# Optimization experiments

Measured on AMD Instinct MI355X. Metric: run time of the kernel, lower is better.

## Reference

```python
import jax, jax.numpy as jnp
import numpy as np

B, S, D = 8, 4096, 1024
H, DH = 16, 64
DM = H * DH  # d_model = 1024


def setup_inputs() -> dict:
    key = jax.random.key(0)
    k0, k1, k2, k3 = jax.random.split(key, 4)
    x = jax.random.uniform(k0, (B, S, D), dtype=jnp.float32)
    # nn.Linear weights (stored here pre-transposed as [in, out]).
    Wq = jax.random.normal(k1, (D, DM), dtype=jnp.float32) * 0.02
    Wkv = jax.random.normal(k2, (D, 2 * DM), dtype=jnp.float32) * 0.02
    Wlin = jax.random.normal(k3, (DM, DM), dtype=jnp.float32) * 0.02
    blin = jnp.zeros((DM,), dtype=jnp.float32)
    return {"x": x, "Wq": Wq, "Wkv": Wkv, "Wlin": Wlin, "blin": blin}


def reference(x, Wq, Wkv, Wlin, blin):
    scale = DH ** (-0.5)
    # projections; cond_dim=None => cond = x (self attention), mask=None
    q = (x @ Wq).reshape(B, S, H, DH)          # [B,S,H,DH]
    kv = (x @ Wkv).reshape(B, S, H, 2 * DH)    # [B,S,H,2*DH]
    k, v = kv[..., :DH], kv[..., DH:]
    # dual softmax: q over feature dim (scaled), k over sequence dim
    q = jax.nn.softmax(q, axis=-1) * scale
    k = jax.nn.softmax(k, axis=1)              # seq axis in BSHD layout
    # context = k^T @ v per (batch, head): [B,H,DH,DH]
    context = jnp.einsum('bshd,bshe->bhde', k, v)
    # out = q @ context: [B,S,H,DH]
    out = jnp.einsum('bshd,bhde->bshe', q, context).reshape(B, S, DM)
    return out @ Wlin + blin
```

## Files before the change

kernel.cpp:

```cpp
#include <hip/hip_runtime.h>
#include <hip/hip_bf16.h>
#include <cstdint>

using bf16 = __hip_bfloat16;
typedef __attribute__((ext_vector_type(8))) short bf16x8;
typedef __attribute__((ext_vector_type(4))) float f32x4;

struct alignas(16) B8 { bf16 h[8]; };
struct alignas(8)  B4 { bf16 h[4]; };

__device__ __forceinline__ void gll16(const void* g, void* l) {
  __builtin_amdgcn_global_load_lds((__attribute__((address_space(1))) void*)g,
                                   (__attribute__((address_space(3))) void*)l,
                                   16, 0, 0);
}

__global__ void cast_f32_bf16(const float* __restrict__ in, bf16* __restrict__ out, long long n) {
  long long i = ((long long)blockIdx.x * blockDim.x + threadIdx.x) * 8;
  if (i >= n) return;
  float4 v0 = *(const float4*)(in + i);
  float4 v1 = *(const float4*)(in + i + 4);
  B8 o;
  o.h[0] = __float2bfloat16(v0.x); o.h[1] = __float2bfloat16(v0.y);
  o.h[2] = __float2bfloat16(v0.z); o.h[3] = __float2bfloat16(v0.w);
  o.h[4] = __float2bfloat16(v1.x); o.h[5] = __float2bfloat16(v1.y);
  o.h[6] = __float2bfloat16(v1.z); o.h[7] = __float2bfloat16(v1.w);
  *(B8*)(out + i) = o;
}

__global__ void tcast(const float* __restrict__ W, bf16* __restrict__ WT, int K, int N) {
  __shared__ float tile[32][33];
  int k0 = blockIdx.y * 32, n0 = blockIdx.x * 32;
  int tx = threadIdx.x, ty = threadIdx.y;
  for (int yy = ty; yy < 32; yy += 8)
    tile[yy][tx] = W[(size_t)(k0 + yy) * N + n0 + tx];
  __syncthreads();
  for (int yy = ty; yy < 32; yy += 8)
    WT[(size_t)(n0 + yy) * K + k0 + tx] = __float2bfloat16(tile[tx][yy]);
}

__device__ __forceinline__ void gemm_mainloop_256(
    const bf16* __restrict__ aop0, const bf16* __restrict__ aop1,
    const bf16* __restrict__ bop0, const bf16* __restrict__ bop1,
    bf16* ldsA, bf16* ldsB, int wd0, int wd1,
    int aoff, int boff, f32x4 (&acc)[8][4])
{
#define STAGE_A(slot, ko) do { gll16(aop0 + (ko), ldsA + (slot) * 8192 + wd0); \
                               gll16(aop1 + (ko), ldsA + (slot) * 8192 + wd1); } while (0)
#define STAGE_B(slot, ko) do { gll16(bop0 + (ko), ldsB + (slot) * 8192 + wd0); \
                               gll16(bop1 + (ko), ldsB + (slot) * 8192 + wd1); } while (0)
#define AFRAG(slot, i) (*(const bf16x8*)(ldsA + (slot) * 8192 + aoff + (i) * 512))
#define BFRAG(slot, j) (*(const bf16x8*)(ldsB + (slot) * 8192 + boff + (j) * 512))

  bf16x8 a1[4], a2[4], bb[2][4];

#define SECTION(S, CURB, NXTB, DO_PF, PFS)                                          \
  do {                                                                              \
    asm volatile("s_waitcnt lgkmcnt(0)" ::: "memory");                              \
    __builtin_amdgcn_sched_barrier(0);                                              \
    __builtin_amdgcn_s_setprio(1);                                                  \
    _Pragma("unroll")                                                               \
    for (int i = 0; i < 4; i++) {                                                   \
      _Pragma("unroll")                                                             \
      for (int j = 0; j < 4; j++)                                                   \
        acc[i][j] = __builtin_amdgcn_mfma_f32_16x16x32_bf16(a1[i], bb[CURB][j],     \
                                                            acc[i][j], 0, 0, 0);    \
      a2[i] = AFRAG(S, i + 4);                                                      \
    }                                                                               \
    asm volatile("s_waitcnt lgkmcnt(0)" ::: "memory");                              \
    __builtin_amdgcn_sched_barrier(0);                                              \
    _Pragma("unroll")                                                               \
    for (int i = 0; i < 4; i++) {                                                   \
      _Pragma("unroll")                                                             \
      for (int j = 0; j < 4; j++)                                                   \
        acc[i + 4][j] = __builtin_amdgcn_mfma_f32_16x16x32_bf16(a2[i], bb[CURB][j], \
                                                                acc[i + 4][j], 0, 0, 0); \
      if (DO_PF) { bb[NXTB][i] = BFRAG(PFS, i); a1[i] = AFRAG(PFS, i); }            \
    }                                                                               \
    __builtin_amdgcn_s_setprio(0);                                                  \
  } while (0)

#define BOUNDARY(VMC, DO_STAGE, SLOT, KO)                                           \
  do {                                                                              \
    asm volatile("s_waitcnt vmcnt(" #VMC ")" ::: "memory");                         \
    __builtin_amdgcn_s_barrier();                                                   \
    __builtin_amdgcn_sched_barrier(0);                                              \
    if (DO_STAGE) { STAGE_A(SLOT, KO); STAGE_B(SLOT, KO); }                         \
  } while (0)

  STAGE_A(0, 0);  STAGE_B(0, 0);
  STAGE_A(1, 32); STAGE_B(1, 32);
  STAGE_A(2, 64); STAGE_B(2, 64);
  asm volatile("s_waitcnt vmcnt(8)" ::: "memory");
  __builtin_amdgcn_s_barrier();
  __builtin_amdgcn_sched_barrier(0);
  STAGE_A(3, 96); STAGE_B(3, 96);
  #pragma unroll
  for (int j = 0; j < 4; j++) bb[0][j] = BFRAG(0, j);
  #pragma unroll
  for (int i = 0; i < 4; i++) a1[i] = AFRAG(0, i);

  for (int q = 0; q < 7; ++q) {
    const int ko = q * 128 + 128;
    SECTION(0, 0, 1, true, 1);
    BOUNDARY(4, true, 0, ko);
    SECTION(1, 1, 0, true, 2);
    BOUNDARY(4, true, 1, ko + 32);
    SECTION(2, 0, 1, true, 3);
    BOUNDARY(4, true, 2, ko + 64);
    SECTION(3, 1, 0, true, 0);
    BOUNDARY(4, true, 3, ko + 96);
  }
  SECTION(0, 0, 1, true, 1);
  BOUNDARY(4, false, 0, 0);
  SECTION(1, 1, 0, true, 2);
  BOUNDARY(0, false, 0, 0);
  SECTION(2, 0, 1, true, 3);
  BOUNDARY(0, false, 0, 0);
  SECTION(3, 1, 0, false, 0);

  __syncthreads();
#undef SECTION
#undef BOUNDARY
#undef STAGE_A
#undef STAGE_B
#undef AFRAG
#undef BFRAG
}

constexpr int QKV_NT = 12;

__global__ __launch_bounds__(512, 2)
void gemm_qkv(const bf16* __restrict__ A, const bf16* __restrict__ BT,
              bf16* __restrict__ Yq, float* __restrict__ ctxAcc)
{
  __shared__ __align__(16) union {
    struct { bf16 a[4 * 8192]; bf16 b[4 * 8192]; } g;
    struct { bf16 ekT[2][16384]; bf16 vT[2][16384]; } c;
  } sm;

  const int t = threadIdx.x;
  const int wave = t >> 6, lane = t & 63;
  const int lr = lane & 15, kq = lane >> 4;
  const int wm = wave >> 2, wn = wave & 3;
  const int bid = (int)blockIdx.x;
  const int swz = (bid & 7) * 192 + (bid >> 3);
  const int bm = swz / QKV_NT, bn = swz % QKV_NT;
  const int m0 = bm * 256, n0 = bn * 256;

  const bf16* aop0 = A + (size_t)(m0 + wave * 16 + lr) * 1024 + kq * 8;
  const bf16* aop1 = A + (size_t)(m0 + 128 + wave * 16 + lr) * 1024 + kq * 8;
  const bf16* bop0 = BT + (size_t)(n0 + wave * 16 + lr) * 1024 + kq * 8;
  const bf16* bop1 = BT + (size_t)(n0 + 128 + wave * 16 + lr) * 1024 + kq * 8;
  const int wd0 = wave * 512;
  const int wd1 = 4096 + wave * 512;

  const int aoff = wm * 4096 + lane * 8;
  const int boff = wn * 2048 + lane * 8;

  const f32x4 zero = {0.f, 0.f, 0.f, 0.f};
  f32x4 acc[8][4];
  #pragma unroll
  for (int i = 0; i < 8; i++)
    #pragma unroll
    for (int j = 0; j < 4; j++) acc[i][j] = zero;

  gemm_mainloop_256(aop0, aop1, bop0, bop1, sm.g.a, sm.g.b, wd0, wd1,
                    aoff, boff, acc);

  if (bn < 4) {
    #pragma unroll
    for (int i = 0; i < 8; i++) {
      #pragma unroll
      for (int r = 0; r < 4; r++) {
        float m = fmaxf(fmaxf(acc[i][0][r], acc[i][1][r]),
                        fmaxf(acc[i][2][r], acc[i][3][r]));
        m = fmaxf(m, __shfl_xor(m, 1));
        m = fmaxf(m, __shfl_xor(m, 2));
        m = fmaxf(m, __shfl_xor(m, 4));
        m = fmaxf(m, __shfl_xor(m, 8));
        float ex[4]; float s = 0.f;
        #pragma unroll
        for (int j = 0; j < 4; j++) { ex[j] = __expf(acc[i][j][r] - m); s += ex[j]; }
        s += __shfl_xor(s, 1);
        s += __shfl_xor(s, 2);
        s += __shfl_xor(s, 4);
        s += __shfl_xor(s, 8);
        const float inv = 0.125f / s;
        const int row = m0 + wm * 128 + i * 16 + kq * 4 + r;
        bf16* yrow = Yq + (size_t)row * 1024 + n0 + wn * 64;
        #pragma unroll
        for (int j = 0; j < 4; j++)
          yrow[j * 16 + lr] = __float2bfloat16(ex[j] * inv);
      }
    }
  } else {
    const int bb2 = m0 >> 12;
    const int h0 = (n0 - 1024) >> 7;
    const int hloc = wn >> 1, isV = wn & 1;
    bf16* const dstT = (isV ? sm.c.vT[hloc] : sm.c.ekT[hloc]);

    float zp[4] = {0.f, 0.f, 0.f, 0.f};
    #pragma unroll
    for (int i = 0; i < 8; i++) {
      const int sbase = wm * 128 + i * 16 + kq * 4;
      const int sxo = sbase >> 3;
      const int sby = (sbase & 7) * 2;
      #pragma unroll
      for (int j = 0; j < 4; j++) {
        const int d = j * 16 + lr;
        B4 pk;
        if (!isV) {
          #pragma unroll
          for (int r = 0; r < 4; r++) {
            float e = __expf(acc[i][j][r]);
            zp[j] += e;
            pk.h[r] = __float2bfloat16(e);
          }
        } else {
          #pragma unroll
          for (int r = 0; r < 4; r++) pk.h[r] = __float2bfloat16(acc[i][j][r]);
        }
        *(B4*)((char*)dstT + d * 512 + ((sxo ^ (d & 7)) << 4) + sby) = pk;
      }
    }

    if (!isV) {
      #pragma unroll
      for (int j = 0; j < 4; j++) {
        zp[j] += __shfl_xor(zp[j], 16);
        zp[j] += __shfl_xor(zp[j], 32);
      }
      if (kq == 0) {
        float* zb = ctxAcc + (size_t)(bb2 * 16 + h0 + hloc) * 4160 + 4096;
        #pragma unroll
        for (int j = 0; j < 4; j++) atomicAdd(zb + j * 16 + lr, zp[j]);
      }
    }
    __syncthreads();

    const int hh = wave >> 2, dq = wave & 3;
    const bf16* const ek = sm.c.ekT[hh];
    const bf16* const vv = sm.c.vT[hh];
    f32x4 racc[4] = {zero, zero, zero, zero};
    #pragma unroll
    for (int ks = 0; ks < 8; ks++) {
      const int ch = ks * 4 + kq;
      bf16x8 af = *(const bf16x8*)((const char*)ek + (dq * 16 + lr) * 512 + ((ch ^ (lr & 7)) << 4));
      #pragma unroll
      for (int j = 0; j < 4; j++) {
        bf16x8 bfr = *(const bf16x8*)((const char*)vv + (j * 16 + lr) * 512 + ((ch ^ (lr & 7)) << 4));
        racc[j] = __builtin_amdgcn_mfma_f32_16x16x32_bf16(af, bfr, racc[j], 0, 0, 0);
      }
    }
    float* cb = ctxAcc + (size_t)(bb2 * 16 + h0 + hh) * 4160;
    #pragma unroll
    for (int j = 0; j < 4; j++) {
      #pragma unroll
      for (int r = 0; r < 4; r++)
        atomicAdd(cb + (dq * 16 + kq * 4 + r) * 64 + j * 16 + lr, racc[j][r]);
    }
  }
}

__global__ __launch_bounds__(256) void make_w2t(const float* __restrict__ ctxAcc,
                                                const bf16* __restrict__ WlinT,
                                                bf16* __restrict__ W2T) {
  const int nc = blockIdx.x;
  const int bh = blockIdx.y;
  const int b = bh >> 4, h = bh & 15;
  const int t = threadIdx.x, lane = t & 63, w = t >> 6;
  const float* src = ctxAcc + (size_t)bh * 4160;
  const float invz = 1.0f / src[4096 + lane];
  float creg[64];
  const float* crow = src + lane * 64;
  #pragma unroll
  for (int e4 = 0; e4 < 16; e4++) {
    float4 v = *(const float4*)(crow + e4 * 4);
    creg[e4 * 4 + 0] = v.x * invz; creg[e4 * 4 + 1] = v.y * invz;
    creg[e4 * 4 + 2] = v.z * invz; creg[e4 * 4 + 3] = v.w * invz;
  }
  for (int i = 0; i < 16; i++) {
    const int n = nc * 64 + w * 16 + i;
    const bf16* wrow = WlinT + (size_t)n * 1024 + h * 64;
    float acc = 0.f;
    #pragma unroll
    for (int e8 = 0; e8 < 8; e8++) {
      B8 v = *(const B8*)(wrow + e8 * 8);
      #pragma unroll
      for (int j = 0; j < 8; j++) acc += creg[e8 * 8 + j] * __bfloat162float(v.h[j]);
    }
    W2T[((size_t)b * 1024 + n) * 1024 + h * 64 + lane] = __float2bfloat16(acc);
  }
}

__global__ __launch_bounds__(512, 2)
void gemm_out(const bf16* __restrict__ Aall, const bf16* __restrict__ BTall,
              float* __restrict__ Call, const float* __restrict__ bias)
{
  __shared__ __align__(16) struct { bf16 a[4 * 8192]; bf16 b[4 * 8192]; } sm;
  const int t = threadIdx.x;
  const int wave = t >> 6, lane = t & 63;
  const int lr = lane & 15, kq = lane >> 4;
  const int wm = wave >> 2, wn = wave & 3;
  const int bid = (int)blockIdx.x;
  const int swz = (bid & 7) * 64 + (bid >> 3);
  const int bz = swz >> 6;
  const int r  = swz & 63;
  const int bm = r >> 2, bn = r & 3;
  const int m0 = bm * 256, n0 = bn * 256;
  const bf16* A  = Aall  + (size_t)bz * 4096 * 1024;
  const bf16* BT = BTall + (size_t)bz * 1024 * 1024;
  float* C       = Call  + (size_t)bz * 4096 * 1024;

  const bf16* aop0 = A + (size_t)(m0 + wave * 16 + lr) * 1024 + kq * 8;
  const bf16* aop1 = A + (size_t)(m0 + 128 + wave * 16 + lr) * 1024 + kq * 8;
  const bf16* bop0 = BT + (size_t)(n0 + wave * 16 + lr) * 1024 + kq * 8;
  const bf16* bop1 = BT + (size_t)(n0 + 128 + wave * 16 + lr) * 1024 + kq * 8;
  const int wd0 = wave * 512;
  const int wd1 = 4096 + wave * 512;

  const int aoff = wm * 4096 + lane * 8;
  const int boff = wn * 2048 + lane * 8;

  const f32x4 zero = {0.f, 0.f, 0.f, 0.f};
  f32x4 acc[8][4];
  #pragma unroll
  for (int i = 0; i < 8; i++)
    #pragma unroll
    for (int j = 0; j < 4; j++) acc[i][j] = zero;

  gemm_mainloop_256(aop0, aop1, bop0, bop1, sm.a, sm.b, wd0, wd1,
                    aoff, boff, acc);

  float bv[4];
  #pragma unroll
  for (int j = 0; j < 4; j++) bv[j] = bias[n0 + wn * 64 + j * 16 + lr];
  #pragma unroll
  for (int i = 0; i < 8; i++) {
    const int row0 = m0 + wm * 128 + i * 16 + kq * 4;
    #pragma unroll
    for (int j = 0; j < 4; j++) {
      const int col = n0 + wn * 64 + j * 16 + lr;
      const float bvj = bv[j];
      #pragma unroll
      for (int r2 = 0; r2 < 4; r2++)
        C[(size_t)(row0 + r2) * 1024 + col] = acc[i][j][r2] + bvj;
    }
  }
}

extern "C" void kernel_launch(void* const* d_in, const int* in_sizes, int n_in,
                              void* d_out, int out_size, void* d_ws, size_t ws_size,
                              hipStream_t stream) {
  (void)in_sizes; (void)n_in; (void)out_size; (void)ws_size;
  const float* x    = (const float*)d_in[0];
  const float* Wq   = (const float*)d_in[1];
  const float* Wkv  = (const float*)d_in[2];
  const float* Wlin = (const float*)d_in[3];
  const float* blin = (const float*)d_in[4];
  float* out = (float*)d_out;

  bf16* x_bf  = (bf16*)d_ws;
  bf16* WTc   = x_bf + 33554432;
  bf16* WlinT = WTc + 3145728;
  bf16* Yq    = WlinT + 1048576;
  bf16* W2T   = Yq + 33554432;
  float* ctxAcc = (float*)(W2T + 8388608);

  cast_f32_bf16<<<16384, 256, 0, stream>>>(x, x_bf, 33554432LL);
  tcast<<<dim3(32, 32), dim3(32, 8), 0, stream>>>(Wq, WTc, 1024, 1024);
  tcast<<<dim3(64, 32), dim3(32, 8), 0, stream>>>(Wkv, WTc + 1048576, 1024, 2048);
  tcast<<<dim3(32, 32), dim3(32, 8), 0, stream>>>(Wlin, WlinT, 1024, 1024);

  hipMemsetAsync(ctxAcc, 0, (size_t)128 * 4160 * sizeof(float), stream);

  gemm_qkv<<<dim3(128 * QKV_NT), 512, 0, stream>>>(x_bf, WTc, Yq, ctxAcc);
  make_w2t<<<dim3(16, 128), 256, 0, stream>>>(ctxAcc, WlinT, W2T);
  gemm_out<<<dim3(512), 512, 0, stream>>>(Yq, W2T, out, blin);
}
```

Before: 419.5 us.

## Store GEMM operands in MFMA fragment-tiled layout for contiguous LDS staging

The bf16 copies of x, the QKV weights, Yq and the fused W2T operand are now written in a fragment-major tiled layout (16-row by 8-element blocks), so each wave's global_load_lds reads one contiguous 1 KB chunk instead of 16 strided rows. The cast kernels become LDS-transposing tile kernels, and the softmax-q and make_w2t epilogues write into the same tiled layout. The aim is better coalescing and fewer memory transactions in both GEMM mainloops. In exchange, the prep kernels are more complex and the q epilogue now does scattered 2-byte stores.

```diff
diff --git a/kernel.cpp b/kernel.cpp
--- a/kernel.cpp
+++ b/kernel.cpp
@@ -15,17 +15,62 @@
                                    16, 0, 0);
 }
 
-__global__ void cast_f32_bf16(const float* __restrict__ in, bf16* __restrict__ out, long long n) {
-  long long i = ((long long)blockIdx.x * blockDim.x + threadIdx.x) * 8;
-  if (i >= n) return;
-  float4 v0 = *(const float4*)(in + i);
-  float4 v1 = *(const float4*)(in + i + 4);
-  B8 o;
-  o.h[0] = __float2bfloat16(v0.x); o.h[1] = __float2bfloat16(v0.y);
-  o.h[2] = __float2bfloat16(v0.z); o.h[3] = __float2bfloat16(v0.w);
-  o.h[4] = __float2bfloat16(v1.x); o.h[5] = __float2bfloat16(v1.y);
-  o.h[6] = __float2bfloat16(v1.z); o.h[7] = __float2bfloat16(v1.w);
-  *(B8*)(out + i) = o;
+
+__global__ __launch_bounds__(256) void cast_x_frag(const float* __restrict__ x,
+                                                   bf16* __restrict__ xr) {
+  __shared__ float tile[16][257];
+  const int g = blockIdx.x;
+  const int t = threadIdx.x;
+  const float* src = x + (size_t)g * 16384;
+  bf16* dst = xr + (size_t)g * 16384;
+  for (int kp = 0; kp < 4; ++kp) {
+    const int k0 = kp * 256;
+    if (kp) __syncthreads();
+    {
+      const int r = t >> 4, cl = t & 15;
+      #pragma unroll
+      for (int s = 0; s < 16; ++s)
+        tile[r][cl + 16 * s] = src[(size_t)r * 1024 + k0 + cl + 16 * s];
+    }
+    __syncthreads();
+    #pragma unroll
+    for (int rd = 0; rd < 2; ++rd) {
+      const int c = rd * 256 + t;
+      const int ql = c >> 4, r = c & 15;
+      B8 o;
+      #pragma unroll
+      for (int jj = 0; jj < 8; ++jj) o.h[jj] = __float2bfloat16(tile[r][ql * 8 + jj]);
+      *(B8*)(dst + ((size_t)(kp * 32 + ql) * 16 + r) * 8) = o;
+    }
+  }
+}
+
+__global__ __launch_bounds__(256) void wcast_frag(const float* __restrict__ W,
+                                                  bf16* __restrict__ out,
+                                                  int N, int n_glob0) {
+  __shared__ float tw[256][17];
+  const int k0 = blockIdx.x * 256;
+  const int n0 = blockIdx.y * 16;
+  const int t = threadIdx.x;
+  {
+    const int nn = t & 15, kk0 = t >> 4;
+    #pragma unroll
+    for (int s = 0; s < 16; ++s) {
+      const int kk = kk0 + 16 * s;
+      tw[kk][nn] = W[(size_t)(k0 + kk) * N + n0 + nn];
+    }
+  }
+  __syncthreads();
+  const int ng = (n_glob0 + n0) >> 4;
+  #pragma unroll
+  for (int rd = 0; rd < 2; ++rd) {
+    const int c = rd * 256 + t;
+    const int ql = c >> 4, r = c & 15;
+    B8 o;
+    #pragma unroll
+    for (int jj = 0; jj < 8; ++jj) o.h[jj] = __float2bfloat16(tw[ql * 8 + jj][r]);
+    *(B8*)(out + (((size_t)ng * 128 + (k0 >> 3) + ql) * 16 + r) * 8) = o;
+  }
 }
 
 __global__ void tcast(const float* __restrict__ W, bf16* __restrict__ WT, int K, int N) {
@@ -45,10 +90,10 @@
     bf16* ldsA, bf16* ldsB, int wd0, int wd1,
     int aoff, int boff, f32x4 (&acc)[8][4])
 {
-#define STAGE_A(slot, ko) do { gll16(aop0 + (ko), ldsA + (slot) * 8192 + wd0); \
-                               gll16(aop1 + (ko), ldsA + (slot) * 8192 + wd1); } while (0)
-#define STAGE_B(slot, ko) do { gll16(bop0 + (ko), ldsB + (slot) * 8192 + wd0); \
-                               gll16(bop1 + (ko), ldsB + (slot) * 8192 + wd1); } while (0)
+#define STAGE_A(slot, ko) do { gll16(aop0 + (ko) * 16, ldsA + (slot) * 8192 + wd0); \
+                               gll16(aop1 + (ko) * 16, ldsA + (slot) * 8192 + wd1); } while (0)
+#define STAGE_B(slot, ko) do { gll16(bop0 + (ko) * 16, ldsB + (slot) * 8192 + wd0); \
+                               gll16(bop1 + (ko) * 16, ldsB + (slot) * 8192 + wd1); } while (0)
 #define AFRAG(slot, i) (*(const bf16x8*)(ldsA + (slot) * 8192 + aoff + (i) * 512))
 #define BFRAG(slot, j) (*(const bf16x8*)(ldsB + (slot) * 8192 + boff + (j) * 512))
 
@@ -148,10 +193,10 @@
   const int bm = swz / QKV_NT, bn = swz % QKV_NT;
   const int m0 = bm * 256, n0 = bn * 256;
 
-  const bf16* aop0 = A + (size_t)(m0 + wave * 16 + lr) * 1024 + kq * 8;
-  const bf16* aop1 = A + (size_t)(m0 + 128 + wave * 16 + lr) * 1024 + kq * 8;
-  const bf16* bop0 = BT + (size_t)(n0 + wave * 16 + lr) * 1024 + kq * 8;
-  const bf16* bop1 = BT + (size_t)(n0 + 128 + wave * 16 + lr) * 1024 + kq * 8;
+  const bf16* aop0 = A + (size_t)((m0 >> 4) + wave) * 16384 + lane * 8;
+  const bf16* aop1 = aop0 + 131072;
+  const bf16* bop0 = BT + (size_t)((n0 >> 4) + wave) * 16384 + lane * 8;
+  const bf16* bop1 = bop0 + 131072;
   const int wd0 = wave * 512;
   const int wd1 = 4096 + wave * 512;
 
@@ -169,6 +214,8 @@
                     aoff, boff, acc);
 
   if (bn < 4) {
+    const int qb = (n0 + wn * 64) >> 3;
+    const int jo = (lr >> 3) * 128;
     #pragma unroll
     for (int i = 0; i < 8; i++) {
       #pragma unroll
@@ -188,10 +235,10 @@
         s += __shfl_xor(s, 8);
         const float inv = 0.125f / s;
         const int row = m0 + wm * 128 + i * 16 + kq * 4 + r;
-        bf16* yrow = Yq + (size_t)row * 1024 + n0 + wn * 64;
+        bf16* yb = Yq + (((size_t)(row >> 4) * 128 + qb) * 16 + (row & 15)) * 8 + (lr & 7);
         #pragma unroll
         for (int j = 0; j < 4; j++)
-          yrow[j * 16 + lr] = __float2bfloat16(ex[j] * inv);
+          yb[j * 256 + jo] = __float2bfloat16(ex[j] * inv);
       }
     }
   } else {
@@ -290,7 +337,9 @@
       #pragma unroll
       for (int j = 0; j < 8; j++) acc += creg[e8 * 8 + j] * __bfloat162float(v.h[j]);
     }
-    W2T[((size_t)b * 1024 + n) * 1024 + h * 64 + lane] = __float2bfloat16(acc);
+    W2T[(size_t)b * 1048576 +
+        (((size_t)(n >> 4) * 128 + h * 8 + (lane >> 3)) * 16 + (n & 15)) * 8 + (lane & 7)]
+        = __float2bfloat16(acc);
   }
 }
 
@@ -309,14 +358,14 @@
   const int r  = swz & 63;
   const int bm = r >> 2, bn = r & 3;
   const int m0 = bm * 256, n0 = bn * 256;
-  const bf16* A  = Aall  + (size_t)bz * 4096 * 1024;
-  const bf16* BT = BTall + (size_t)bz * 1024 * 1024;
-  float* C       = Call  + (size_t)bz * 4096 * 1024;
-
-  const bf16* aop0 = A + (size_t)(m0 + wave * 16 + lr) * 1024 + kq * 8;
-  const bf16* aop1 = A + (size_t)(m0 + 128 + wave * 16 + lr) * 1024 + kq * 8;
-  const bf16* bop0 = BT + (size_t)(n0 + wave * 16 + lr) * 1024 + kq * 8;
-  const bf16* bop1 = BT + (size_t)(n0 + 128 + wave * 16 + lr) * 1024 + kq * 8;
+  const bf16* A  = Aall  + (size_t)bz * 4194304;
+  const bf16* BT = BTall + (size_t)bz * 1048576;
+  float* C       = Call  + (size_t)bz * 4194304;
+
+  const bf16* aop0 = A + (size_t)((m0 >> 4) + wave) * 16384 + lane * 8;
+  const bf16* aop1 = aop0 + 131072;
+  const bf16* bop0 = BT + (size_t)((n0 >> 4) + wave) * 16384 + lane * 8;
+  const bf16* bop1 = bop0 + 131072;
   const int wd0 = wave * 512;
   const int wd1 = 4096 + wave * 512;
 
@@ -368,9 +417,9 @@
   bf16* W2T   = Yq + 33554432;
   float* ctxAcc = (float*)(W2T + 8388608);
 
-  cast_f32_bf16<<<16384, 256, 0, stream>>>(x, x_bf, 33554432LL);
-  tcast<<<dim3(32, 32), dim3(32, 8), 0, stream>>>(Wq, WTc, 1024, 1024);
-  tcast<<<dim3(64, 32), dim3(32, 8), 0, stream>>>(Wkv, WTc + 1048576, 1024, 2048);
+  cast_x_frag<<<2048, 256, 0, stream>>>(x, x_bf);
+  wcast_frag<<<dim3(4, 64), 256, 0, stream>>>(Wq, WTc, 1024, 0);
+  wcast_frag<<<dim3(4, 128), 256, 0, stream>>>(Wkv, WTc, 2048, 1024);
   tcast<<<dim3(32, 32), dim3(32, 8), 0, stream>>>(Wlin, WlinT, 1024, 1024);
 
   hipMemsetAsync(ctxAcc, 0, (size_t)128 * 4160 * sizeof(float), stream);
```

Result: faster. 372.6 us (-11.2%).
